# Kernel optimization log

Hardware: AMD Instinct MI355X
Metric: run time of the kernel (lower is better)

## Reference

```python
import jax, jax.numpy as jnp
import numpy as np

N_NODES = 500_000
N_EDGES = 16_000_000


def setup_inputs() -> dict:
    key = jax.random.key(0)
    ks = jax.random.split(key, 8)
    x = jax.random.normal(ks[0], (N_NODES, 10), dtype=jnp.float32)
    edge_index = jax.random.randint(ks[1], (2, N_EDGES), 0, N_NODES, dtype=jnp.int32)
    # PyG-style init scale ~ 1/sqrt(fan_in)
    Wl1 = jax.random.normal(ks[2], (5, 10), dtype=jnp.float32) / np.sqrt(10)
    Wr1 = jax.random.normal(ks[3], (5, 10), dtype=jnp.float32) / np.sqrt(10)
    b1 = jnp.zeros((5,), jnp.float32)
    Wl_mid = jax.random.normal(ks[4], (8, 5, 5), dtype=jnp.float32) / np.sqrt(5)
    Wr_mid = jax.random.normal(ks[5], (8, 5, 5), dtype=jnp.float32) / np.sqrt(5)
    b_mid = jnp.zeros((8, 5), jnp.float32)
    Wl10 = jax.random.normal(ks[6], (1, 5), dtype=jnp.float32) / np.sqrt(5)
    Wr10 = jax.random.normal(ks[7], (1, 5), dtype=jnp.float32) / np.sqrt(5)
    b10 = jnp.zeros((1,), jnp.float32)
    return dict(x=x, edge_index=edge_index, Wl1=Wl1, Wr1=Wr1, b1=b1,
                Wl_mid=Wl_mid, Wr_mid=Wr_mid, b_mid=b_mid,
                Wl10=Wl10, Wr10=Wr10, b10=b10)


def _mean_aggregate(h, src, dst):
    # scatter-mean of source features onto destination nodes
    s = jax.ops.segment_sum(h[src], dst, num_segments=N_NODES)
    cnt = jax.ops.segment_sum(jnp.ones((src.shape[0], 1), h.dtype), dst,
                              num_segments=N_NODES)
    return s / jnp.maximum(cnt, 1.0)


def _sage_conv(h, src, dst, Wl, Wr, b):
    # out = lin_l(mean_neighbors) + lin_r(h); bias belongs to lin_l (PyG default)
    agg = _mean_aggregate(h, src, dst)
    return agg @ Wl.T + h @ Wr.T + b


def reference(x, edge_index, Wl1, Wr1, b1, Wl_mid, Wr_mid, b_mid, Wl10, Wr10, b10):
    src, dst = edge_index[0], edge_index[1]
    h = jax.nn.relu(_sage_conv(x, src, dst, Wl1, Wr1, b1))

    def step(h, layer_params):
        Wl, Wr, b = layer_params
        h = jax.nn.relu(_sage_conv(h, src, dst, Wl, Wr, b))
        return h, None

    h, _ = jax.lax.scan(step, h, (Wl_mid, Wr_mid, b_mid))
    out = _sage_conv(h, src, dst, Wl10, Wr10, b10)  # [N, 1], no relu on last
    return out
```

## Files before the change

### kernel.cpp

```cpp
#include <hip/hip_runtime.h>

constexpr int NN = 500000;
constexpr int NE = 16000000;
constexpr int BN = 512;
constexpr int NBUCK = (NN + BN - 1) / BN;
constexpr int NSLICE = 8;
constexpr int NKEY = NSLICE * BN;
constexpr int CAPA = 17408;
constexpr int TILE_A = 16384;
constexpr int NTILE_A = (NE + TILE_A - 1) / TILE_A;
constexpr int NB_NODE = (NN + 255) / 256;

typedef int int4v __attribute__((ext_vector_type(4)));

__device__ __forceinline__ unsigned bfr(float x) {
    unsigned u = __float_as_uint(x);
    u += 0x7fffu + ((u >> 16) & 1u);
    return u >> 16;
}
__device__ __forceinline__ float bfl(unsigned u) { return __uint_as_float(u << 16); }
__device__ __forceinline__ float bfh(unsigned u) { return __uint_as_float(u & 0xffff0000u); }

__global__ void __launch_bounds__(1024, 8) passA(const int* __restrict__ src,
                                                 const int* __restrict__ dst,
                                                 int* __restrict__ gcnt,
                                                 int* __restrict__ storeA) {
    __shared__ int hist[1024];
    __shared__ int lbase[1024];
    __shared__ int lcur[1024];
    __shared__ int gbase[1024];
    __shared__ int stage[TILE_A];
    const int tid = threadIdx.x;
    const int base = blockIdx.x * TILE_A;
    const int nt = min(TILE_A, NE - base);
    hist[tid] = 0;
    __syncthreads();
    for (int i = tid; i < nt; i += 1024)
        atomicAdd(&hist[dst[base + i] >> 9], 1);
    __syncthreads();
    const int cnt = hist[tid];
    lbase[tid] = cnt;
    __syncthreads();
    for (int off = 1; off < 1024; off <<= 1) {
        int add = (tid >= off) ? lbase[tid - off] : 0;
        __syncthreads();
        lbase[tid] += add;
        __syncthreads();
    }
    const int lb = lbase[tid] - cnt;
    lcur[tid] = lb;
    if (tid < NBUCK && cnt > 0) {
        int g = atomicAdd(&gcnt[tid], cnt);
        gbase[tid] = tid * CAPA + g;
    }
    __syncthreads();
    lbase[tid] = lb;
    for (int i = tid; i < nt; i += 1024) {
        int d = dst[base + i];
        int s = src[base + i];
        int p = atomicAdd(&lcur[d >> 9], 1);
        stage[p] = (s << 9) | (d & 511);
    }
    __syncthreads();
    const int wid = tid >> 6, lane = tid & 63;
    for (int b = wid; b < NBUCK; b += 16) {
        int c = hist[b];
        if (c == 0) continue;
        int l0 = lbase[b];
        int g0 = gbase[b];
        int wl = min(c, (b + 1) * CAPA - g0);
        for (int j = lane; j < wl; j += 64)
            storeA[g0 + j] = stage[l0 + j];
    }
}

__global__ void __launch_bounds__(512) passB(const int* __restrict__ gcnt,
                                             const int* __restrict__ storeA,
                                             int* __restrict__ sortedB,
                                             float* __restrict__ inv,
                                             int* __restrict__ soff) {
    __shared__ int hist[NKEY];
    __shared__ int sc[512];
    __shared__ int stage[CAPA];
    const int bkt = blockIdx.x;
    const int tid = threadIdx.x;
#pragma unroll
    for (int u = 0; u < NKEY / 512; ++u) hist[tid + u * 512] = 0;
    __syncthreads();
    const int n = min(gcnt[bkt], CAPA);
    const int* bs = storeA + (size_t)bkt * CAPA;
    const int n4 = n & ~3;
    for (int k = tid * 4; k < n4; k += 2048) {
        int4v e4 = *(const int4v*)(bs + k);
#pragma unroll
        for (int u = 0; u < 4; ++u) {
            int e = e4[u];
            int key = ((e >> 26) << 10) | ((e & 511) << 1) | ((e >> 25) & 1);
            atomicAdd(&hist[key], 1);
        }
    }
    for (int k = n4 + tid; k < n; k += 512) {
        int e = bs[k];
        int key = ((e >> 26) << 10) | ((e & 511) << 1) | ((e >> 25) & 1);
        atomicAdd(&hist[key], 1);
    }
    __syncthreads();
    {
        int node = bkt * BN + tid;
        if (node < NN) {
            int c = 0;
#pragma unroll
            for (int p = 0; p < 4; ++p)
#pragma unroll
                for (int q = 0; q < 2; ++q)
                    c += hist[(p << 10) | (tid << 1) | q];
            inv[node] = 1.0f / fmaxf((float)c, 1.0f);
        }
    }
    int v[NKEY / 512];
    int sum = 0;
#pragma unroll
    for (int u = 0; u < NKEY / 512; ++u) {
        v[u] = hist[tid * (NKEY / 512) + u];
        sum += v[u];
    }
    sc[tid] = sum;
    __syncthreads();
    for (int off = 1; off < 512; off <<= 1) {
        int add = (tid >= off) ? sc[tid - off] : 0;
        __syncthreads();
        sc[tid] += add;
        __syncthreads();
    }
    int run = sc[tid] - sum;
    if ((tid & 127) == 0) soff[bkt * 9 + (tid >> 7)] = bkt * CAPA + run;
    if (tid == 511) soff[bkt * 9 + 4] = bkt * CAPA + n;
#pragma unroll
    for (int u = 0; u < NKEY / 512; ++u) {
        hist[tid * (NKEY / 512) + u] = run;
        run += v[u];
    }
    __syncthreads();
    for (int k = tid * 4; k < n4; k += 2048) {
        int4v e4 = *(const int4v*)(bs + k);
#pragma unroll
        for (int u = 0; u < 4; ++u) {
            int e = e4[u];
            int key = ((e >> 26) << 10) | ((e & 511) << 1) | ((e >> 25) & 1);
            int p = atomicAdd(&hist[key], 1);
            stage[p] = e;
        }
    }
    for (int k = n4 + tid; k < n; k += 512) {
        int e = bs[k];
        int key = ((e >> 26) << 10) | ((e & 511) << 1) | ((e >> 25) & 1);
        int p = atomicAdd(&hist[key], 1);
        stage[p] = e;
    }
    __syncthreads();
    int* ob = sortedB + (size_t)bkt * CAPA;
    for (int k = tid * 4; k < n4; k += 2048)
        *(int4v*)(ob + k) = *(const int4v*)(stage + k);
    for (int k = n4 + tid; k < n; k += 512)
        ob[k] = stage[k];
}

__global__ void __launch_bounds__(256) transform0(const float* __restrict__ x,
                                                  const float* __restrict__ Wl1,
                                                  uint4* __restrict__ t16) {
    int i = blockIdx.x * 256 + threadIdx.x;
    if (i >= NN) return;
    float xi[10];
#pragma unroll
    for (int k = 0; k < 10; ++k) xi[k] = x[i * 10 + k];
    float v[5];
#pragma unroll
    for (int j = 0; j < 5; ++j) {
        float a = 0.f;
#pragma unroll
        for (int k = 0; k < 10; ++k) a += xi[k] * Wl1[j * 10 + k];
        v[j] = a;
    }
    uint4 w;
    w.x = bfr(v[0]) | (bfr(v[1]) << 16);
    w.y = bfr(v[2]) | (bfr(v[3]) << 16);
    w.z = bfr(v[4]);
    w.w = 0;
    t16[i] = w;
}

__device__ __forceinline__ void process_range5_lds(const int* eds,
                                                   int k, const int ke,
                                                   const uint4* __restrict__ t16,
                                                   float* __restrict__ acc) {
    int cur = -1;
    float a0 = 0, a1 = 0, a2 = 0, a3 = 0, a4 = 0;
    auto flush = [&]() {
        if (cur >= 0) {
            float* p = &acc[cur * 5];
            atomicAdd(p + 0, a0); atomicAdd(p + 1, a1); atomicAdd(p + 2, a2);
            atomicAdd(p + 3, a3); atomicAdd(p + 4, a4);
        }
    };
    auto edge = [&](int e, uint4 w) {
        int d = e & 511;
        if (d != cur) { flush(); cur = d; a0 = a1 = a2 = a3 = a4 = 0.f; }
        a0 += bfl(w.x); a1 += bfh(w.x); a2 += bfl(w.y); a3 += bfh(w.y); a4 += bfl(w.z);
    };
    while (k < ke && (k & 3)) {
        int e = eds[k];
        edge(e, t16[e >> 9]);
        ++k;
    }
    for (; k + 7 < ke; k += 8) {
        int4v ea = *(const int4v*)(eds + k);
        int4v eb = *(const int4v*)(eds + k + 4);
        uint4 w0 = t16[ea.x >> 9];
        uint4 w1 = t16[ea.y >> 9];
        uint4 w2 = t16[ea.z >> 9];
        uint4 w3 = t16[ea.w >> 9];
        uint4 w4 = t16[eb.x >> 9];
        uint4 w5 = t16[eb.y >> 9];
        uint4 w6 = t16[eb.z >> 9];
        uint4 w7 = t16[eb.w >> 9];
        edge(ea.x, w0); edge(ea.y, w1); edge(ea.z, w2); edge(ea.w, w3);
        edge(eb.x, w4); edge(eb.y, w5); edge(eb.z, w6); edge(eb.w, w7);
    }
    for (; k + 3 < ke; k += 4) {
        int4v e4 = *(const int4v*)(eds + k);
        uint4 w0 = t16[e4.x >> 9];
        uint4 w1 = t16[e4.y >> 9];
        uint4 w2 = t16[e4.z >> 9];
        uint4 w3 = t16[e4.w >> 9];
        edge(e4.x, w0); edge(e4.y, w1); edge(e4.z, w2); edge(e4.w, w3);
    }
    for (; k < ke; ++k) {
        int e = eds[k];
        edge(e, t16[e >> 9]);
    }
    flush();
}

template <int FIN, int FNEXT>
__global__ void __launch_bounds__(512, 4) layer_fused(const int* __restrict__ soff,
                                                      const int* __restrict__ sorted,
                                                      const uint4* __restrict__ t16,
                                                      const float* __restrict__ hin,
                                                      const float* __restrict__ Wr,
                                                      const float* __restrict__ b,
                                                      const float* __restrict__ Wln,
                                                      const float* __restrict__ inv,
                                                      float* __restrict__ hout,
                                                      uint4* __restrict__ tn16,
                                                      float* __restrict__ tnP) {
    __shared__ float acc[BN * 5];
    __shared__ int eds[CAPA];
    const int bkt = blockIdx.x;
    const int tid = threadIdx.x;
    const int base = bkt * CAPA;
    const int n = soff[bkt * 9 + 4] - base;
    for (int k = tid; k < BN * 5; k += 512) acc[k] = 0.f;
    const int n4 = n & ~3;
    for (int k = tid * 4; k < n4; k += 2048)
        *(int4v*)(eds + k) = __builtin_nontemporal_load((const int4v*)(sorted + base + k));
    for (int k = n4 + tid; k < n; k += 512)
        eds[k] = sorted[base + k];
    __syncthreads();
#pragma unroll
    for (int p = 0; p < 4; ++p) {
        int beg = soff[bkt * 9 + p] - base, end = soff[bkt * 9 + p + 1] - base;
        int c = (end - beg + 511) >> 9;
        int k = beg + tid * c;
        int ke = min(k + c, end);
        if (k < ke) process_range5_lds(eds, k, ke, t16, acc);
        __syncthreads();
    }

    int node = bkt * BN + tid;
    if (node >= NN) return;
    float iv = inv[node];
    float vin[FIN];
#pragma unroll
    for (int kk = 0; kk < FIN; ++kk) vin[kk] = hin[(size_t)node * FIN + kk];
    float ho[5];
#pragma unroll
    for (int jo = 0; jo < 5; ++jo) {
        float v = acc[tid * 5 + jo] * iv + b[jo];
#pragma unroll
        for (int kk = 0; kk < FIN; ++kk) v += vin[kk] * Wr[jo * FIN + kk];
        v = fmaxf(v, 0.f);
        hout[(size_t)node * 5 + jo] = v;
        ho[jo] = v;
    }
    if constexpr (FNEXT == 5) {
        float tv[5];
#pragma unroll
        for (int j2 = 0; j2 < 5; ++j2) {
            float v = 0.f;
#pragma unroll
            for (int jo = 0; jo < 5; ++jo) v += ho[jo] * Wln[j2 * 5 + jo];
            tv[j2] = v;
        }
        uint4 w;
        w.x = bfr(tv[0]) | (bfr(tv[1]) << 16);
        w.y = bfr(tv[2]) | (bfr(tv[3]) << 16);
        w.z = bfr(tv[4]);
        w.w = 0;
        tn16[node] = w;
    } else {
        float v = 0.f;
#pragma unroll
        for (int jo = 0; jo < 5; ++jo) v += ho[jo] * Wln[jo];
        tnP[node] = v;
    }
}

__global__ void __launch_bounds__(512, 4) final_layer(const int* __restrict__ soff,
                                                      const int* __restrict__ sorted,
                                                      const float* __restrict__ t,
                                                      const float* __restrict__ hin,
                                                      const float* __restrict__ Wr,
                                                      const float* __restrict__ b,
                                                      const float* __restrict__ inv,
                                                      float* __restrict__ out) {
    __shared__ float acc[BN];
    __shared__ int eds[CAPA];
    const int bkt = blockIdx.x;
    const int tid = threadIdx.x;
    const int base = bkt * CAPA;
    const int n = soff[bkt * 9 + 4] - base;
    if (tid < BN) acc[tid] = 0.f;
    const int sn4 = n & ~3;
    for (int k = tid * 4; k < sn4; k += 2048)
        *(int4v*)(eds + k) = __builtin_nontemporal_load((const int4v*)(sorted + base + k));
    for (int k = sn4 + tid; k < n; k += 512)
        eds[k] = sorted[base + k];
    __syncthreads();
    int c = (n + 511) >> 9;
    int k = tid * c;
    const int ke = min(k + c, n);
    int cur = -1;
    float a0 = 0.f;
    auto flush = [&]() { if (cur >= 0) atomicAdd(&acc[cur], a0); };
    auto edge = [&](int e, float q) {
        int d = e & 511;
        if (d != cur) { flush(); cur = d; a0 = 0.f; }
        a0 += q;
    };
    int kk = k;
    while (kk < ke && (kk & 3)) { int e = eds[kk]; edge(e, t[e >> 9]); ++kk; }
    for (; kk + 7 < ke; kk += 8) {
        int4v ea = *(const int4v*)(eds + kk);
        int4v eb = *(const int4v*)(eds + kk + 4);
        float q0 = t[ea.x >> 9], q1 = t[ea.y >> 9], q2 = t[ea.z >> 9], q3 = t[ea.w >> 9];
        float q4 = t[eb.x >> 9], q5 = t[eb.y >> 9], q6 = t[eb.z >> 9], q7 = t[eb.w >> 9];
        edge(ea.x, q0); edge(ea.y, q1); edge(ea.z, q2); edge(ea.w, q3);
        edge(eb.x, q4); edge(eb.y, q5); edge(eb.z, q6); edge(eb.w, q7);
    }
    for (; kk + 3 < ke; kk += 4) {
        int4v e4 = *(const int4v*)(eds + kk);
        float q0 = t[e4.x >> 9], q1 = t[e4.y >> 9], q2 = t[e4.z >> 9], q3 = t[e4.w >> 9];
        edge(e4.x, q0); edge(e4.y, q1); edge(e4.z, q2); edge(e4.w, q3);
    }
    for (; kk < ke; ++kk) { int e = eds[kk]; edge(e, t[e >> 9]); }
    flush();
    __syncthreads();
    int node = bkt * BN + tid;
    if (node >= NN) return;
    float v = acc[tid] * inv[node] + b[0];
#pragma unroll
    for (int kq = 0; kq < 5; ++kq) v += hin[(size_t)node * 5 + kq] * Wr[kq];
    out[node] = v;
}

extern "C" void kernel_launch(void* const* d_in, const int* in_sizes, int n_in,
                              void* d_out, int out_size, void* d_ws, size_t ws_size,
                              hipStream_t stream) {
    (void)in_sizes; (void)n_in; (void)out_size; (void)ws_size;
    const float* x    = (const float*)d_in[0];
    const int*   ei   = (const int*)d_in[1];
    const float* Wl1  = (const float*)d_in[2];
    const float* Wr1  = (const float*)d_in[3];
    const float* b1   = (const float*)d_in[4];
    const float* Wlm  = (const float*)d_in[5];
    const float* Wrm  = (const float*)d_in[6];
    const float* bm   = (const float*)d_in[7];
    const float* Wl10 = (const float*)d_in[8];
    const float* Wr10 = (const float*)d_in[9];
    const float* b10  = (const float*)d_in[10];
    float* out = (float*)d_out;

    const int* src = ei;
    const int* dst = ei + NE;

    int* wsI = (int*)d_ws;
    int*   gcnt    = wsI;
    int*   soff    = wsI + 1024;
    int*   sortedB = wsI + 10240;
    float* inv     = (float*)(wsI + 17017856);
    int*   storeA  = wsI + 20019200;
    uint4* tA = (uint4*)(wsI + 20019200);
    uint4* tB = (uint4*)(wsI + 22019200);
    float* tP = (float*)(wsI + 24019200);
    float* hA = (float*)(wsI + 24519424);
    float* hB = (float*)(wsI + 27020032);

    dim3 gb(NBUCK);
    dim3 tb(512);

    hipMemsetAsync(gcnt, 0, 1024 * sizeof(int), stream);
    passA<<<dim3(NTILE_A), dim3(1024), 0, stream>>>(src, dst, gcnt, storeA);
    passB<<<gb, tb, 0, stream>>>(gcnt, storeA, sortedB, inv, soff);

    transform0<<<dim3(NB_NODE), dim3(256), 0, stream>>>(x, Wl1, tA);
    layer_fused<10, 5><<<gb, tb, 0, stream>>>(soff, sortedB, tA,
                                              x, Wr1, b1, Wlm, inv, hA, tB, nullptr);

    const uint4* tcur = tB; uint4* tnxt = tA;
    const float* hcur = hA; float* hnext = hB;
    for (int mi = 0; mi < 7; ++mi) {
        layer_fused<5, 5><<<gb, tb, 0, stream>>>(soff, sortedB, tcur,
                                                 hcur, Wrm + mi * 25, bm + mi * 5,
                                                 Wlm + (mi + 1) * 25, inv, hnext,
                                                 tnxt, nullptr);
        const uint4* tt = tcur; tcur = tnxt; tnxt = (uint4*)tt;
        const float* th = hcur; hcur = hnext; hnext = (float*)th;
    }
    layer_fused<5, 1><<<gb, tb, 0, stream>>>(soff, sortedB, tcur,
                                             hcur, Wrm + 7 * 25, bm + 7 * 5,
                                             Wl10, inv, hnext, nullptr, tP);
    final_layer<<<gb, tb, 0, stream>>>(soff, sortedB, tP, hnext, Wr10, b10, inv, out);
}
```

Before: 1.579 ms.

## Stage edges per pass in smaller LDS buffer to raise occupancy

The fused layer kernel no longer copies a whole bucket's edge list into a large shared array up front. It loads each of the four sub-pass slices into a smaller buffer capped at PAIR_CAP entries, synchronising before and after each pass, and raises the launch-bounds occupancy hint. The smaller LDS footprint should let more blocks share a CU and hide gather latency better. The 8-wide unrolled gather loops are also dropped in favour of 4-wide ones. The cost is scalar rather than vector global loads, extra barriers, and silent truncation if any pass slice exceeds the cap.

Measured after the change: 1.558 ms. Within noise of the previous version (-1.4%).

```diff
diff --git a/kernel.cpp b/kernel.cpp
--- a/kernel.cpp
+++ b/kernel.cpp
@@ -7,6 +7,7 @@
 constexpr int NSLICE = 8;
 constexpr int NKEY = NSLICE * BN;
 constexpr int CAPA = 17408;
+constexpr int PAIR_CAP = 5120;
 constexpr int TILE_A = 16384;
 constexpr int NTILE_A = (NE + TILE_A - 1) / TILE_A;
 constexpr int NB_NODE = (NN + 255) / 256;
@@ -212,20 +213,6 @@
         edge(e, t16[e >> 9]);
         ++k;
     }
-    for (; k + 7 < ke; k += 8) {
-        int4v ea = *(const int4v*)(eds + k);
-        int4v eb = *(const int4v*)(eds + k + 4);
-        uint4 w0 = t16[ea.x >> 9];
-        uint4 w1 = t16[ea.y >> 9];
-        uint4 w2 = t16[ea.z >> 9];
-        uint4 w3 = t16[ea.w >> 9];
-        uint4 w4 = t16[eb.x >> 9];
-        uint4 w5 = t16[eb.y >> 9];
-        uint4 w6 = t16[eb.z >> 9];
-        uint4 w7 = t16[eb.w >> 9];
-        edge(ea.x, w0); edge(ea.y, w1); edge(ea.z, w2); edge(ea.w, w3);
-        edge(eb.x, w4); edge(eb.y, w5); edge(eb.z, w6); edge(eb.w, w7);
-    }
     for (; k + 3 < ke; k += 4) {
         int4v e4 = *(const int4v*)(eds + k);
         uint4 w0 = t16[e4.x >> 9];
@@ -242,7 +229,7 @@
 }
 
 template <int FIN, int FNEXT>
-__global__ void __launch_bounds__(512, 4) layer_fused(const int* __restrict__ soff,
+__global__ void __launch_bounds__(512, 8) layer_fused(const int* __restrict__ soff,
                                                       const int* __restrict__ sorted,
                                                       const uint4* __restrict__ t16,
                                                       const float* __restrict__ hin,
@@ -254,24 +241,21 @@
                                                       uint4* __restrict__ tn16,
                                                       float* __restrict__ tnP) {
     __shared__ float acc[BN * 5];
-    __shared__ int eds[CAPA];
+    __shared__ int eds[PAIR_CAP];
     const int bkt = blockIdx.x;
     const int tid = threadIdx.x;
-    const int base = bkt * CAPA;
-    const int n = soff[bkt * 9 + 4] - base;
     for (int k = tid; k < BN * 5; k += 512) acc[k] = 0.f;
-    const int n4 = n & ~3;
-    for (int k = tid * 4; k < n4; k += 2048)
-        *(int4v*)(eds + k) = __builtin_nontemporal_load((const int4v*)(sorted + base + k));
-    for (int k = n4 + tid; k < n; k += 512)
-        eds[k] = sorted[base + k];
-    __syncthreads();
 #pragma unroll
     for (int p = 0; p < 4; ++p) {
-        int beg = soff[bkt * 9 + p] - base, end = soff[bkt * 9 + p + 1] - base;
-        int c = (end - beg + 511) >> 9;
-        int k = beg + tid * c;
-        int ke = min(k + c, end);
+        const int beg = soff[bkt * 9 + p];
+        const int n = min(soff[bkt * 9 + p + 1] - beg, PAIR_CAP);
+#pragma unroll 4
+        for (int k = tid; k < n; k += 512)
+            eds[k] = __builtin_nontemporal_load(sorted + beg + k);
+        __syncthreads();
+        const int c = (n + 511) >> 9;
+        const int k = tid * c;
+        const int ke = min(k + c, n);
         if (k < ke) process_range5_lds(eds, k, ke, t16, acc);
         __syncthreads();
     }
@@ -349,14 +333,6 @@
     };
     int kk = k;
     while (kk < ke && (kk & 3)) { int e = eds[kk]; edge(e, t[e >> 9]); ++kk; }
-    for (; kk + 7 < ke; kk += 8) {
-        int4v ea = *(const int4v*)(eds + kk);
-        int4v eb = *(const int4v*)(eds + kk + 4);
-        float q0 = t[ea.x >> 9], q1 = t[ea.y >> 9], q2 = t[ea.z >> 9], q3 = t[ea.w >> 9];
-        float q4 = t[eb.x >> 9], q5 = t[eb.y >> 9], q6 = t[eb.z >> 9], q7 = t[eb.w >> 9];
-        edge(ea.x, q0); edge(ea.y, q1); edge(ea.z, q2); edge(ea.w, q3);
-        edge(eb.x, q4); edge(eb.y, q5); edge(eb.z, q6); edge(eb.w, q7);
-    }
     for (; kk + 3 < ke; kk += 4) {
         int4v e4 = *(const int4v*)(eds + kk);
         float q0 = t[e4.x >> 9], q1 = t[e4.y >> 9], q2 = t[e4.z >> 9], q3 = t[e4.w >> 9];
```
